# Optimization experiments

Measured on AMD Instinct MI355X. Metric: run time of the kernel, lower is better.

The kernel has to match this reference:

```python
import jax, jax.numpy as jnp
import numpy as np

IMG_W, IMG_H = 960.0, 512.0          # NETWORK.IMAGE_SIZE
HM_W, HM_H = 240.0, 128.0            # NETWORK.HEATMAP_SIZE (w, h)
GRID_SIZE = (8000.0, 8000.0, 2000.0)
CUBE = (80, 80, 20)
SPACE_CENTER = (0.0, -500.0, 800.0)


def _make_grid():
    # compute_grid: meshgrid(indexing='ij'), flattened to [nbins, 3]
    gx = np.linspace(-GRID_SIZE[0] / 2, GRID_SIZE[0] / 2, CUBE[0]) + SPACE_CENTER[0]
    gy = np.linspace(-GRID_SIZE[1] / 2, GRID_SIZE[1] / 2, CUBE[1]) + SPACE_CENTER[1]
    gz = np.linspace(-GRID_SIZE[2] / 2, GRID_SIZE[2] / 2, CUBE[2]) + SPACE_CENTER[2]
    X, Y, Z = np.meshgrid(gx, gy, gz, indexing='ij')
    return jnp.asarray(np.stack([X.ravel(), Y.ravel(), Z.ravel()], 1), jnp.float32)


def setup_inputs() -> dict:
    key = jax.random.key(0)
    ks = jax.random.split(key, 8)
    n, B, J, H, W = 5, 4, 15, 128, 240
    heatmaps = jax.random.uniform(ks[0], (n, B, J, H, W), jnp.float32)
    # cameras: rotate about z per view, positioned so all grid points have depth > 0
    thetas = np.linspace(0.0, 2 * np.pi, n, endpoint=False)
    Rs = np.zeros((n, B, 3, 3), np.float32)
    for v, th in enumerate(thetas):
        c, s = np.cos(th), np.sin(th)
        Rs[v, :] = np.array([[c, -s, 0.0], [s, c, 0.0], [0.0, 0.0, 1.0]], np.float32)
    cam_R = jnp.asarray(Rs)
    cam_T = jnp.asarray(np.tile(np.array([0.0, 0.0, -5000.0], np.float32), (n, B, 1))) \
        + 50.0 * jax.random.normal(ks[1], (n, B, 3), jnp.float32)
    cam_f = 1500.0 + 20.0 * jax.random.normal(ks[2], (n, B, 2), jnp.float32)
    cam_c = jnp.asarray([IMG_W / 2, IMG_H / 2], jnp.float32) \
        + 5.0 * jax.random.normal(ks[3], (n, B, 2), jnp.float32)
    cam_k = jnp.asarray(np.tile(np.array([-0.01, 0.001, 0.0], np.float32), (n, B, 1))) \
        + 1e-4 * jax.random.normal(ks[4], (n, B, 3), jnp.float32)
    cam_p = 1e-3 * jax.random.normal(ks[5], (n, B, 2), jnp.float32)
    center = jnp.asarray([IMG_W / 2, IMG_H / 2], jnp.float32) \
        + 10.0 * jax.random.normal(ks[6], (n, B, 2), jnp.float32)
    scale = jnp.asarray([IMG_W / 200.0, IMG_H / 200.0], jnp.float32) \
        * (1.0 + 0.05 * jax.random.uniform(ks[7], (n, B, 2), jnp.float32))
    return {"heatmaps": heatmaps, "cam_R": cam_R, "cam_T": cam_T, "cam_f": cam_f,
            "cam_c": cam_c, "cam_k": cam_k, "cam_p": cam_p, "center": center,
            "scale": scale}


def _forward(heatmaps, cam_R, cam_T, cam_f, cam_c, cam_k, cam_p, center, scale):
    n, B, J, Hd, Wd = heatmaps.shape
    grid = _make_grid()                                   # [N, 3]
    N = grid.shape[0]
    # --- project_pose (pinhole + radial/tangential distortion) ---
    diff = grid[None, None] - cam_T[:, :, None, :]        # [v,b,N,3]
    xcam = jnp.einsum('vbij,vbnj->vbni', cam_R, diff)     # [v,b,N,3]
    y = xcam[..., :2] / (xcam[..., 2:3] + 1e-5)
    r2 = jnp.sum(y * y, -1)                               # [v,b,N]
    radial = 1.0 + cam_k[..., 0:1] * r2 + cam_k[..., 1:2] * r2 ** 2 + cam_k[..., 2:3] * r2 ** 3
    tan = cam_p[..., 0:1] * y[..., 1] + cam_p[..., 1:2] * y[..., 0]
    y = y * (radial + 2.0 * tan)[..., None] \
        + jnp.stack([cam_p[..., 1], cam_p[..., 0]], -1)[:, :, None, :] * r2[..., None]
    pix = cam_f[:, :, None, :] * y + cam_c[:, :, None, :]  # [v,b,N,2]
    # --- bounding: inside image of size (width, height) = 2*center ---
    wh = 2.0 * center                                      # [v,b,2]
    bounding = ((pix[..., 0] >= 0) & (pix[..., 1] >= 0)
                & (pix[..., 0] < wh[..., 0:1]) & (pix[..., 1] < wh[..., 1:2])
                ).astype(heatmaps.dtype)                   # [v,b,N]
    maxwh = jnp.maximum(wh[..., 0], wh[..., 1])[..., None, None]
    pix = jnp.clip(pix, -1.0, maxwh)
    # --- get_transform(center, scale, 0, img_size) + do_transform ---
    hs = 200.0 * scale                                     # [v,b,2]
    img = jnp.asarray([IMG_W, IMG_H], heatmaps.dtype)
    t_scale = img / hs                                     # diag of affine
    t_off = img * (-center / hs + 0.5)
    xy = pix * t_scale[:, :, None, :] + t_off[:, :, None, :]
    # scale to heatmap resolution, then to normalized [-1,1] (align_corners=True)
    xy = xy * (jnp.asarray([HM_W, HM_H], heatmaps.dtype) / img)
    sg = xy / jnp.asarray([HM_W - 1, HM_H - 1], heatmaps.dtype) * 2.0 - 1.0
    sg = jnp.clip(sg, -1.1, 1.1)
    # --- bilinear grid_sample, align_corners=True, zeros padding ---
    px = (sg[..., 0] + 1.0) * 0.5 * (Wd - 1)
    py = (sg[..., 1] + 1.0) * 0.5 * (Hd - 1)
    x0 = jnp.floor(px)
    y0 = jnp.floor(py)
    wx = px - x0
    wy = py - y0
    x0i = x0.astype(jnp.int32)
    y0i = y0.astype(jnp.int32)
    flat = heatmaps.reshape(n, B, J, Hd * Wd)

    def corner(xi, yi):
        valid = ((xi >= 0) & (xi < Wd) & (yi >= 0) & (yi < Hd)).astype(heatmaps.dtype)
        idx = jnp.clip(yi, 0, Hd - 1) * Wd + jnp.clip(xi, 0, Wd - 1)   # [v,b,N]
        g = jnp.take_along_axis(flat, idx[:, :, None, :], axis=3)       # [v,b,J,N]
        return g * valid[:, :, None, :]

    val = (corner(x0i, y0i) * ((1 - wx) * (1 - wy))[:, :, None, :]
           + corner(x0i + 1, y0i) * (wx * (1 - wy))[:, :, None, :]
           + corner(x0i, y0i + 1) * ((1 - wx) * wy)[:, :, None, :]
           + corner(x0i + 1, y0i + 1) * (wx * wy)[:, :, None, :])       # [v,b,J,N]
    # --- per-view cube = bounding * sampled; combine over views ---
    cubes_v = bounding[:, :, None, :] * val
    num = jnp.sum(cubes_v * bounding[:, :, None, :], axis=0)            # [b,J,N]
    den = jnp.sum(bounding, axis=0)[:, None, :] + 1e-6
    cubes = jnp.clip(num / den, 0.0, 1.0).reshape(B, J, CUBE[0], CUBE[1], CUBE[2])
    grids = jnp.broadcast_to(grid, (B, N, 3))
    return cubes, grids


def reference(heatmaps, cam_R, cam_T, cam_f, cam_c, cam_k, cam_p, center, scale):
    return _forward(heatmaps, cam_R, cam_T, cam_f, cam_c, cam_k, cam_p, center, scale)
```

## Files before the change

### kernel.cpp

```cpp
#include <hip/hip_runtime.h>

#define NV 5
#define NB 4
#define NJ 15
#define HD 128
#define WD 240
#define CX 80
#define CY 80
#define CZ 20
#define NPTS (CX*CY*CZ)
#define BLOCKS_PER_B (NPTS/256)
#define NWG (NB*BLOCKS_PER_B)

struct ViewSample {
    float w[4];
    int   cx0, cx1, cy0, cy1;
    float bnd;
};

__device__ __forceinline__ ViewSample project_one_view(
    float gx, float gy, float gz,
    const float* __restrict__ cam_R, const float* __restrict__ cam_T,
    const float* __restrict__ cam_f, const float* __restrict__ cam_c,
    const float* __restrict__ cam_k, const float* __restrict__ cam_p,
    const float* __restrict__ center, const float* __restrict__ scale,
    int cb)
{
    const float* R = cam_R + cb*9;
    const float* T = cam_T + cb*3;
    float fx = cam_f[cb*2+0], fy = cam_f[cb*2+1];
    float ccx = cam_c[cb*2+0], ccy = cam_c[cb*2+1];
    float k0 = cam_k[cb*3+0], k1 = cam_k[cb*3+1], k2 = cam_k[cb*3+2];
    float p0 = cam_p[cb*2+0], p1 = cam_p[cb*2+1];
    float cenx = center[cb*2+0], ceny = center[cb*2+1];
    float scx = scale[cb*2+0],  scy = scale[cb*2+1];

    float dx = gx - T[0], dy = gy - T[1], dz = gz - T[2];
    float xc = R[0]*dx + R[1]*dy + R[2]*dz;
    float yc = R[3]*dx + R[4]*dy + R[5]*dz;
    float zc = R[6]*dx + R[7]*dy + R[8]*dz;
    float invz = 1.0f / (zc + 1e-5f);
    float ux = xc * invz, uy = yc * invz;
    float r2 = ux*ux + uy*uy;
    float radial = 1.0f + k0*r2 + k1*(r2*r2) + k2*(r2*r2*r2);
    float tn = p0*uy + p1*ux;
    float m  = radial + 2.0f*tn;
    float xd = ux*m + p1*r2;
    float yd = uy*m + p0*r2;
    float pixx = fx*xd + ccx;
    float pixy = fy*yd + ccy;

    float whx = 2.0f*cenx, why = 2.0f*ceny;
    float bnd = (pixx >= 0.0f && pixy >= 0.0f && pixx < whx && pixy < why) ? 1.0f : 0.0f;
    float mwh = fmaxf(whx, why);
    pixx = fminf(fmaxf(pixx, -1.0f), mwh);
    pixy = fminf(fmaxf(pixy, -1.0f), mwh);

    float hsx = 200.0f*scx, hsy = 200.0f*scy;
    float xyx = (pixx * (960.0f/hsx) + 960.0f*(-cenx/hsx + 0.5f)) * 0.25f;
    float xyy = (pixy * (512.0f/hsy) + 512.0f*(-ceny/hsy + 0.5f)) * 0.25f;
    float sgx = (xyx / 239.0f) * 2.0f - 1.0f;
    float sgy = (xyy / 127.0f) * 2.0f - 1.0f;
    sgx = fminf(fmaxf(sgx, -1.1f), 1.1f);
    sgy = fminf(fmaxf(sgy, -1.1f), 1.1f);

    float pxf = (sgx + 1.0f) * 0.5f * 239.0f;
    float pyf = (sgy + 1.0f) * 0.5f * 127.0f;
    float x0f = floorf(pxf), y0f = floorf(pyf);
    float wx = pxf - x0f, wy = pyf - y0f;
    int x0 = (int)x0f, y0 = (int)y0f;
    int x1 = x0 + 1,   y1 = y0 + 1;
    float vx0 = (x0 >= 0 && x0 < WD) ? 1.0f : 0.0f;
    float vx1 = (x1 >= 0 && x1 < WD) ? 1.0f : 0.0f;
    float vy0 = (y0 >= 0 && y0 < HD) ? 1.0f : 0.0f;
    float vy1 = (y1 >= 0 && y1 < HD) ? 1.0f : 0.0f;

    ViewSample s;
    s.cx0 = min(max(x0, 0), WD-1);
    s.cx1 = min(max(x1, 0), WD-1);
    s.cy0 = min(max(y0, 0), HD-1);
    s.cy1 = min(max(y1, 0), HD-1);
    s.w[0] = (1.0f-wx)*(1.0f-wy) * vx0*vy0 * bnd;
    s.w[1] = wx*(1.0f-wy)        * vx1*vy0 * bnd;
    s.w[2] = (1.0f-wx)*wy        * vx0*vy1 * bnd;
    s.w[3] = wx*wy               * vx1*vy1 * bnd;
    s.bnd = bnd;
    return s;
}

__device__ __forceinline__ void grid_coords(int nn, float& gx, float& gy, float& gz) {
    int iz = nn % CZ;
    int iy = (nn / CZ) % CY;
    int ix = nn / (CZ*CY);
    gx = (float)(((double)ix * (8000.0/79.0) - 4000.0) + 0.0);
    gy = (float)(((double)iy * (8000.0/79.0) - 4000.0) - 500.0);
    gz = (float)(((double)iz * (2000.0/19.0) - 1000.0) + 800.0);
}

__global__ __launch_bounds__(256) void project_kernel_fused(
    const float* __restrict__ hm,
    const float* __restrict__ cam_R, const float* __restrict__ cam_T,
    const float* __restrict__ cam_f, const float* __restrict__ cam_c,
    const float* __restrict__ cam_k, const float* __restrict__ cam_p,
    const float* __restrict__ center, const float* __restrict__ scale,
    float* __restrict__ out_cubes, float* __restrict__ out_grids)
{
    int wg   = (int)blockIdx.x;
    int swz  = (wg % 8) * (NWG/8) + wg / 8;
    const int b  = swz / BLOCKS_PER_B;
    const int nn = (swz % BLOCKS_PER_B)*256 + threadIdx.x;

    float gx, gy, gz;
    grid_coords(nn, gx, gy, gz);

    float acc[NJ];
    #pragma unroll
    for (int j = 0; j < NJ; ++j) acc[j] = 0.0f;
    float den = 0.0f;

    #pragma unroll 1
    for (int v = 0; v < NV; ++v) {
        int cb = v*NB + b;
        ViewSample s = project_one_view(gx, gy, gz, cam_R, cam_T, cam_f, cam_c,
                                        cam_k, cam_p, center, scale, cb);
        den += s.bnd;
        float wsum = s.w[0] + s.w[1] + s.w[2] + s.w[3];
        if (__any(wsum > 0.0f)) {
            if (wsum > 0.0f) {
                int o00 = s.cy0*WD + s.cx0;
                int o10 = s.cy0*WD + s.cx1;
                int o01 = s.cy1*WD + s.cx0;
                int o11 = s.cy1*WD + s.cx1;
                const float* base = hm + (size_t)cb*NJ*(HD*WD);
                #pragma unroll
                for (int j = 0; j < NJ; ++j) {
                    const float* p = base + (size_t)j*(HD*WD);
                    acc[j] += s.w[0]*p[o00] + s.w[1]*p[o10]
                            + s.w[2]*p[o01] + s.w[3]*p[o11];
                }
            }
        }
    }

    float inv_den = 1.0f / (den + 1e-6f);
    #pragma unroll
    for (int j = 0; j < NJ; ++j) {
        float val = fminf(fmaxf(acc[j]*inv_den, 0.0f), 1.0f);
        out_cubes[((size_t)b*NJ + j)*NPTS + nn] = val;
    }
    float* g = out_grids + ((size_t)b*NPTS + nn)*3;
    g[0] = gx; g[1] = gy; g[2] = gz;
}

extern "C" void kernel_launch(void* const* d_in, const int* in_sizes, int n_in,
                              void* d_out, int out_size, void* d_ws, size_t ws_size,
                              hipStream_t stream) {
    const float* hm     = (const float*)d_in[0];
    const float* cam_R  = (const float*)d_in[1];
    const float* cam_T  = (const float*)d_in[2];
    const float* cam_f  = (const float*)d_in[3];
    const float* cam_c  = (const float*)d_in[4];
    const float* cam_k  = (const float*)d_in[5];
    const float* cam_p  = (const float*)d_in[6];
    const float* center = (const float*)d_in[7];
    const float* scale  = (const float*)d_in[8];

    float* out_cubes = (float*)d_out;
    float* out_grids = out_cubes + (size_t)NB*NJ*NPTS;

    hipLaunchKernelGGL(project_kernel_fused,
                       dim3(NWG), dim3(256), 0, stream,
                       hm, cam_R, cam_T, cam_f, cam_c, cam_k, cam_p,
                       center, scale, out_cubes, out_grids);
}
```

Measured before the change: 147.6 us.

## Split views across wavefronts and reduce per-view accumulators through LDS

Each block now handles 64 grid points with five wavefronts, one per camera view, in place of one thread looping serially over all five views. Each wavefront projects and bilinearly samples its own view, writes per-joint partial sums to shared memory, and after a barrier every wave reduces and stores three joints. The goal is more parallelism and memory-level parallelism on the gathers, since the view loop was serial. The cost is more threads doing the grid-coordinate work redundantly, a shared-memory round trip, and a block barrier.

```diff
diff --git a/kernel.cpp b/kernel.cpp
--- a/kernel.cpp
+++ b/kernel.cpp
@@ -9,8 +9,9 @@
 #define CY 80
 #define CZ 20
 #define NPTS (CX*CY*CZ)
-#define BLOCKS_PER_B (NPTS/256)
-#define NWG (NB*BLOCKS_PER_B)
+#define PTS_PER_BLK 64
+#define CHUNKS (NPTS/PTS_PER_BLK)
+#define NWG2 (NB*CHUNKS)
 
 struct ViewSample {
     float w[4];
@@ -97,7 +98,7 @@
     gz = (float)(((double)iz * (2000.0/19.0) - 1000.0) + 800.0);
 }
 
-__global__ __launch_bounds__(256) void project_kernel_fused(
+__global__ __launch_bounds__(320) void project_kernel_split_direct(
     const float* __restrict__ hm,
     const float* __restrict__ cam_R, const float* __restrict__ cam_T,
     const float* __restrict__ cam_f, const float* __restrict__ cam_c,
@@ -105,25 +106,31 @@
     const float* __restrict__ center, const float* __restrict__ scale,
     float* __restrict__ out_cubes, float* __restrict__ out_grids)
 {
-    int wg   = (int)blockIdx.x;
-    int swz  = (wg % 8) * (NWG/8) + wg / 8;
-    const int b  = swz / BLOCKS_PER_B;
-    const int nn = (swz % BLOCKS_PER_B)*256 + threadIdx.x;
+    __shared__ float lds_acc[NJ][NV][PTS_PER_BLK];
+    __shared__ float lds_den[NV][PTS_PER_BLK];
+
+    int wg  = (int)blockIdx.x;
+    int swz = (wg % 8) * (NWG2/8) + wg / 8;
+    const int b     = swz / CHUNKS;
+    const int chunk = swz % CHUNKS;
+    const int n0    = chunk * PTS_PER_BLK;
+
+    const int w    = threadIdx.x >> 6;
+    const int lane = threadIdx.x & 63;
+    const int nn   = n0 + lane;
 
     float gx, gy, gz;
     grid_coords(nn, gx, gy, gz);
 
-    float acc[NJ];
-    #pragma unroll
-    for (int j = 0; j < NJ; ++j) acc[j] = 0.0f;
-    float den = 0.0f;
-
-    #pragma unroll 1
-    for (int v = 0; v < NV; ++v) {
-        int cb = v*NB + b;
+    {
+        const int v  = w;
+        const int cb = v*NB + b;
         ViewSample s = project_one_view(gx, gy, gz, cam_R, cam_T, cam_f, cam_c,
                                         cam_k, cam_p, center, scale, cb);
-        den += s.bnd;
+        float acc[NJ];
+        #pragma unroll
+        for (int j = 0; j < NJ; ++j) acc[j] = 0.0f;
+
         float wsum = s.w[0] + s.w[1] + s.w[2] + s.w[3];
         if (__any(wsum > 0.0f)) {
             if (wsum > 0.0f) {
@@ -140,16 +147,32 @@
                 }
             }
         }
+        #pragma unroll
+        for (int j = 0; j < NJ; ++j) lds_acc[j][v][lane] = acc[j];
+        lds_den[v][lane] = s.bnd;
     }
 
-    float inv_den = 1.0f / (den + 1e-6f);
-    #pragma unroll
-    for (int j = 0; j < NJ; ++j) {
-        float val = fminf(fmaxf(acc[j]*inv_den, 0.0f), 1.0f);
-        out_cubes[((size_t)b*NJ + j)*NPTS + nn] = val;
+    __syncthreads();
+
+    {
+        float den = lds_den[0][lane] + lds_den[1][lane] + lds_den[2][lane]
+                  + lds_den[3][lane] + lds_den[4][lane];
+        float inv = 1.0f / (den + 1e-6f);
+        int j0 = 3*w;
+        #pragma unroll
+        for (int jj = 0; jj < 3; ++jj) {
+            int j = j0 + jj;
+            float sv = lds_acc[j][0][lane] + lds_acc[j][1][lane]
+                     + lds_acc[j][2][lane] + lds_acc[j][3][lane]
+                     + lds_acc[j][4][lane];
+            float val = fminf(fmaxf(sv * inv, 0.0f), 1.0f);
+            out_cubes[((size_t)b*NJ + j)*NPTS + nn] = val;
+        }
+        if (w == 0) {
+            float* g = out_grids + ((size_t)b*NPTS + nn)*3;
+            g[0] = gx; g[1] = gy; g[2] = gz;
+        }
     }
-    float* g = out_grids + ((size_t)b*NPTS + nn)*3;
-    g[0] = gx; g[1] = gy; g[2] = gz;
 }
 
 extern "C" void kernel_launch(void* const* d_in, const int* in_sizes, int n_in,
@@ -168,8 +191,8 @@
     float* out_cubes = (float*)d_out;
     float* out_grids = out_cubes + (size_t)NB*NJ*NPTS;
 
-    hipLaunchKernelGGL(project_kernel_fused,
-                       dim3(NWG), dim3(256), 0, stream,
+    hipLaunchKernelGGL(project_kernel_split_direct,
+                       dim3(NWG2), dim3(320), 0, stream,
                        hm, cam_R, cam_T, cam_f, cam_c, cam_k, cam_p,
                        center, scale, out_cubes, out_grids);
 }
```

New measurement: 137.6 us. -6.7%, faster.
